# Kernel tuning notes

Hardware: AMD Instinct MI355X
Metric: run time of the kernel (lower is better)

The kernel has to match this reference:

```python
import jax, jax.numpy as jnp
import numpy as np

T, B, H, L = 1024, 64, 512, 2  # seq_len, batch, hidden(=input), num_layers


def setup_inputs() -> dict:
    key = jax.random.key(0)
    ks = jax.random.split(key, 9)
    std = 1.0 / np.sqrt(H)

    def u(k, shape):
        return jax.random.uniform(k, shape, jnp.float32, -std, std)

    x = jax.random.normal(ks[0], (T, B, H), jnp.float32)
    # per-direction stacked params: weights [L, 4H, in], biases [L, 4H]
    Wxh_f = u(ks[1], (L, 4 * H, H)); bxh_f = u(ks[2], (L, 4 * H))
    Whh_f = u(ks[3], (L, 4 * H, H)); bhh_f = u(ks[4], (L, 4 * H))
    Wxh_b = u(ks[5], (L, 4 * H, H)); bxh_b = u(ks[6], (L, 4 * H))
    Whh_b = u(ks[7], (L, 4 * H, H)); bhh_b = u(ks[8], (L, 4 * H))
    # LSTMCell.reset_parameters sets forget-gate bias chunk to 1/H
    fg = 1.0 / H
    bxh_f = bxh_f.at[:, H:2 * H].set(fg); bhh_f = bhh_f.at[:, H:2 * H].set(fg)
    bxh_b = bxh_b.at[:, H:2 * H].set(fg); bhh_b = bhh_b.at[:, H:2 * H].set(fg)
    return {"x": x,
            "Wxh_f": Wxh_f, "bxh_f": bxh_f, "Whh_f": Whh_f, "bhh_f": bhh_f,
            "Wxh_b": Wxh_b, "bxh_b": bxh_b, "Whh_b": Whh_b, "bhh_b": bhh_b}


def _run_direction(x, Wxh, bxh, Whh, bhh, reverse):
    # x: [T, B, in]; stacked L-layer LSTM scan in one direction.
    seq = x
    hs, cs = [], []
    for l in range(L):
        Wx, bx, Wh, bh = Wxh[l], bxh[l], Whh[l], bhh[l]

        def step(carry, xt):
            h, c = carry
            g = xt @ Wx.T + bx + h @ Wh.T + bh  # [B, 4H]
            i, f, gc, o = jnp.split(g, 4, axis=-1)  # chunk order: i, f, c, o
            c2 = jax.nn.sigmoid(f) * c + jax.nn.sigmoid(i) * jnp.tanh(gc)
            h2 = jax.nn.sigmoid(o) * jnp.tanh(c2)
            return (h2, c2), h2

        z = jnp.zeros((x.shape[1], H), x.dtype)
        (h, c), seq = jax.lax.scan(step, (z, z), seq, reverse=reverse)
        hs.append(h); cs.append(c)
    return seq, jnp.stack(hs), jnp.stack(cs)  # [T,B,H], [L,B,H], [L,B,H]


def reference(x, Wxh_f, bxh_f, Whh_f, bhh_f, Wxh_b, bxh_b, Whh_b, bhh_b):
    out_f, h_f, c_f = _run_direction(x, Wxh_f, bxh_f, Whh_f, bhh_f, reverse=False)
    out_b, h_b, c_b = _run_direction(x, Wxh_b, bxh_b, Whh_b, bhh_b, reverse=True)
    output = jnp.concatenate([out_f, out_b], axis=-1)  # [T, B, 2H]
    hidden = jnp.concatenate([h_f, h_b], axis=0)       # [2L, B, H]
    cell = jnp.concatenate([c_f, c_b], axis=0)         # [2L, B, H]
    return (output, hidden, cell)
```

## Files before the change

kernel.cpp:

```cpp
#include <hip/hip_runtime.h>
#include <hip/hip_bf16.h>


typedef __hip_bfloat16 bf16;
typedef short bf16x8 __attribute__((ext_vector_type(8)));
typedef float f32x4 __attribute__((ext_vector_type(4)));
typedef unsigned long long u64;

constexpr int T = 1024, B = 64, H = 512, G4 = 2048;
constexpr int W = 16;
constexpr int NW = 64;
constexpr int FSTRIDE = 16;
constexpr int ESTRIDE = 16;
constexpr size_t OUT_ELEMS = (size_t)T * B * 1024;
constexpr size_t HID_OFF   = OUT_ELEMS;
constexpr size_t CELL_OFF  = OUT_ELEMS + (size_t)4 * B * H;

__device__ __align__(256) unsigned g_flags[4 * NW * FSTRIDE];
__device__ __align__(256) unsigned g_epoch[4 * ESTRIDE];
__device__ __align__(256) bf16 g_ring [2 * W * B * H];
__device__ __align__(256) bf16 g_ring2[2 * W * B * H];

__global__ void init_ctrs() {
  const int i = blockIdx.x * blockDim.x + threadIdx.x;
  if (i < 4 * NW * FSTRIDE) g_flags[i] = 0;
  if (i < 4 * ESTRIDE)      g_epoch[i] = 0;
}

__device__ __forceinline__ bf16x8 cvt8(const float* p) {
  const float4 u = *(const float4*)p;
  const float4 v = *(const float4*)(p + 4);
  union { bf16 h[8]; bf16x8 r; } o;
  o.h[0] = __float2bfloat16(u.x); o.h[1] = __float2bfloat16(u.y);
  o.h[2] = __float2bfloat16(u.z); o.h[3] = __float2bfloat16(u.w);
  o.h[4] = __float2bfloat16(v.x); o.h[5] = __float2bfloat16(v.y);
  o.h[6] = __float2bfloat16(v.z); o.h[7] = __float2bfloat16(v.w);
  return o.r;
}

__device__ __forceinline__ bf16x8 ld16_dev(const bf16* p) {
  union { u64 u[2]; bf16x8 v; } r;
  r.u[0] = __hip_atomic_load((const u64*)p,     __ATOMIC_RELAXED,
                             __HIP_MEMORY_SCOPE_AGENT);
  r.u[1] = __hip_atomic_load((const u64*)p + 1, __ATOMIC_RELAXED,
                             __HIP_MEMORY_SCOPE_AGENT);
  return r.v;
}

__device__ __forceinline__ void st2_dev(bf16* p, float x) {
  const bf16 h = (bf16)x;
  unsigned short u;
  __builtin_memcpy(&u, &h, 2);
  __hip_atomic_store((unsigned short*)p, u, __ATOMIC_RELAXED,
                     __HIP_MEMORY_SCOPE_AGENT);
}

__device__ __forceinline__ void wave_poll(const unsigned* base, int lane,
                                          unsigned tgt) {
  const unsigned* p = base + lane * FSTRIDE;
  for (;;) {
    unsigned v = __hip_atomic_load(p, __ATOMIC_RELAXED,
                                   __HIP_MEMORY_SCOPE_AGENT);
    if (__all((int)(v >= tgt))) break;
    __builtin_amdgcn_s_sleep(1);
  }
}

__device__ __forceinline__ void poll_ge(const unsigned* p, unsigned tgt) {
  while (__hip_atomic_load(p, __ATOMIC_RELAXED,
                           __HIP_MEMORY_SCOPE_AGENT) < tgt)
    __builtin_amdgcn_s_sleep(1);
}

__global__ void __launch_bounds__(256, 1)
lstm_bidir(const float* __restrict__ x,
           const float* Wxf, const float* bxf, const float* Whf, const float* bhf,
           const float* Wxb, const float* bxb, const float* Whb, const float* bhb,
           float* out)
{
  __shared__ bf16 Wl[32 * 1024];

  const int tid   = threadIdx.x;
  const int bid   = blockIdx.x;
  const int stage = bid & 3;
  const int wg    = bid >> 2;
  const int dir   = stage & 1;
  const int layer = stage >> 1;
  const int c0    = wg * 8;

  const float* Wx = dir ? Wxb : Wxf;
  const float* Wh = dir ? Whb : Whf;
  const float* bx = dir ? bxb : bxf;
  const float* bh = dir ? bhb : bhf;
  bf16* ring  = g_ring  + (size_t)dir * W * B * H;
  bf16* ring2 = g_ring2 + (size_t)dir * W * B * H;

  for (int c = tid; c < 32 * 128; c += 256) {
    const int n  = c >> 7;
    const int kb = c & 127;
    const int ke = kb * 8;
    const int j = n >> 2, g = n & 3;
    const size_t row = (size_t)layer * G4 + (size_t)g * H + (c0 + j);
    const float* src = (ke < H) ? (Wx + row * H + ke) : (Wh + row * H + (ke - H));
    bf16x8 wv = cvt8(src);
    *(bf16x8*)(Wl + n * 1024 + ((kb ^ (n & 7)) * 8)) = wv;
  }

  const int lane = tid & 63, wi = tid >> 6;
  const int quad = lane >> 4, mr = lane & 15;
  const int g2 = wi & 1;
  const int mh = wi >> 1;
  const int nb = g2 * 16 + mr;
  const int j  = nb >> 2, gg = nb & 3;
  const int sw = nb & 7;

  const size_t brow = (size_t)layer * G4 + (size_t)gg * H + (c0 + j);
  const float bias = bx[brow] + bh[brow];

  __syncthreads();

  float cst[2][4] = {};
  unsigned nrounds = 0;
  unsigned*       myflags   = g_flags + stage * NW * FSTRIDE;
  unsigned*       myepoch   = g_epoch + stage * ESTRIDE;
  const unsigned* prodepoch = g_epoch + dir * ESTRIDE;
  const unsigned* consepoch = g_epoch + (2 + dir) * ESTRIDE;

  const int r0 = (stage < 2) ? 0 : 1;
  for (int r = r0; r < r0 + T; ++r) {
    int t;
    if (stage == 0)      t = r;
    else if (stage == 1) t = (T - 1) - r;
    else if (stage == 2) t = r - 1;
    else                 t = T - r;

    const bool first = dir ? (t == T - 1) : (t == 0);
    const bool last  = dir ? (t == 0) : (t == T - 1);

    const float* xf = nullptr;
    const bf16 *xsb = nullptr;
    const bf16 *hsrc; bf16* hdst_bf; float* hdst_f32 = nullptr;
    if (stage < 2) {
      xf      = x    + (size_t)t * B * H;
      hsrc    = ring + (size_t)((r - 1) & (W - 1)) * B * H;
      hdst_bf = ring + (size_t)(r & (W - 1)) * B * H;
    } else {
      xsb      = ring  + (size_t)((r - 1) & (W - 1)) * B * H;
      hsrc     = ring2 + (size_t)((r - 1) & (W - 1)) * B * H;
      hdst_bf  = ring2 + (size_t)(r & (W - 1)) * B * H;
      hdst_f32 = out + (size_t)t * B * 1024 + (size_t)dir * H;
    }

    f32x4 acc0 = {0.f, 0.f, 0.f, 0.f};
    f32x4 acc1 = {0.f, 0.f, 0.f, 0.f};
    const int arow = mh * 32 + mr;

    if (stage < 2) {
      #pragma unroll
      for (int kk = 0; kk < 16; ++kk) {
        const int blk = kk * 4 + quad;
        bf16x8 bfr = *(const bf16x8*)(Wl + nb * 1024 + ((blk ^ sw) * 8));
        const float* ap = xf + (size_t)arow * H + blk * 8;
        bf16x8 a0 = cvt8(ap);
        bf16x8 a1 = cvt8(ap + (size_t)16 * H);
        acc0 = __builtin_amdgcn_mfma_f32_16x16x32_bf16(a0, bfr, acc0, 0, 0, 0);
        acc1 = __builtin_amdgcn_mfma_f32_16x16x32_bf16(a1, bfr, acc1, 0, 0, 0);
      }
      if (tid < 64) {
        if (wg == 0) {
          wave_poll(myflags, tid, nrounds);
          if (tid == 0) {
            __hip_atomic_store(myepoch, nrounds, __ATOMIC_RELAXED,
                               __HIP_MEMORY_SCOPE_AGENT);
            if (r >= W) poll_ge(consepoch, (unsigned)(r - W + 1));
          }
        } else if (tid == 0) {
          poll_ge(myepoch, nrounds);
          if (r >= W) poll_ge(consepoch, (unsigned)(r - W + 1));
        }
      }
      __syncthreads();
      if (!first) {
        #pragma unroll
        for (int kk = 0; kk < 16; ++kk) {
          const int blk = 64 + kk * 4 + quad;
          bf16x8 bfr = *(const bf16x8*)(Wl + nb * 1024 + ((blk ^ sw) * 8));
          const bf16* ap = hsrc + (size_t)arow * H + (kk * 4 + quad) * 8;
          bf16x8 a0 = ld16_dev(ap);
          bf16x8 a1 = ld16_dev(ap + (size_t)16 * H);
          acc0 = __builtin_amdgcn_mfma_f32_16x16x32_bf16(a0, bfr, acc0, 0, 0, 0);
          acc1 = __builtin_amdgcn_mfma_f32_16x16x32_bf16(a1, bfr, acc1, 0, 0, 0);
        }
      }
    } else {
      if (tid == 0) poll_ge(prodepoch, (unsigned)r);
      __syncthreads();
      #pragma unroll
      for (int kk = 0; kk < 16; ++kk) {
        const int blk = kk * 4 + quad;
        bf16x8 bfr = *(const bf16x8*)(Wl + nb * 1024 + ((blk ^ sw) * 8));
        const bf16* ap = xsb + (size_t)arow * H + blk * 8;
        bf16x8 a0 = ld16_dev(ap);
        bf16x8 a1 = ld16_dev(ap + (size_t)16 * H);
        acc0 = __builtin_amdgcn_mfma_f32_16x16x32_bf16(a0, bfr, acc0, 0, 0, 0);
        acc1 = __builtin_amdgcn_mfma_f32_16x16x32_bf16(a1, bfr, acc1, 0, 0, 0);
      }
      if (tid < 64) {
        if (wg == 0) {
          wave_poll(myflags, tid, nrounds);
          if (tid == 0)
            __hip_atomic_store(myepoch, nrounds, __ATOMIC_RELAXED,
                               __HIP_MEMORY_SCOPE_AGENT);
        } else if (tid == 0) {
          poll_ge(myepoch, nrounds);
        }
      }
      __syncthreads();
      if (!first) {
        #pragma unroll
        for (int kk = 0; kk < 16; ++kk) {
          const int blk = 64 + kk * 4 + quad;
          bf16x8 bfr = *(const bf16x8*)(Wl + nb * 1024 + ((blk ^ sw) * 8));
          const bf16* ap = hsrc + (size_t)arow * H + (kk * 4 + quad) * 8;
          bf16x8 a0 = ld16_dev(ap);
          bf16x8 a1 = ld16_dev(ap + (size_t)16 * H);
          acc0 = __builtin_amdgcn_mfma_f32_16x16x32_bf16(a0, bfr, acc0, 0, 0, 0);
          acc1 = __builtin_amdgcn_mfma_f32_16x16x32_bf16(a1, bfr, acc1, 0, 0, 0);
        }
      }
    }

    #pragma unroll
    for (int m = 0; m < 2; ++m) {
      const f32x4 av = m ? acc1 : acc0;
      #pragma unroll
      for (int rr = 0; rr < 4; ++rr) {
        const float v  = av[rr] + bias;
        const float v1 = __shfl_xor(v, 1);
        const float v2 = __shfl_xor(v, 2);
        const float v3 = __shfl_xor(v, 3);
        float gi, gf, gc, go;
        if (gg == 0)      { gi = v;  gf = v1; gc = v2; go = v3; }
        else if (gg == 1) { gi = v1; gf = v;  gc = v3; go = v2; }
        else if (gg == 2) { gi = v2; gf = v3; gc = v;  go = v1; }
        else              { gi = v3; gf = v2; gc = v1; go = v;  }
        const float si = 1.f / (1.f + __expf(-gi));
        const float sf = 1.f / (1.f + __expf(-gf));
        const float so = 1.f / (1.f + __expf(-go));
        const float tc = 1.f - 2.f / (1.f + __expf(2.f * gc));
        const float c2 = sf * cst[m][rr] + si * tc;
        cst[m][rr] = c2;
        const float th = 1.f - 2.f / (1.f + __expf(2.f * c2));
        const float hv = so * th;
        if (gg == 0) {
          const int b = mh * 32 + m * 16 + quad * 4 + rr;
          st2_dev(hdst_bf + (size_t)b * H + (c0 + j), hv);
          if (stage >= 2) hdst_f32[(size_t)b * 1024 + (c0 + j)] = hv;
          if (last) {
            const size_t p = (size_t)(dir * 2 + layer) * (B * H) + (size_t)b * H + (c0 + j);
            out[HID_OFF + p]  = hv;
            out[CELL_OFF + p] = c2;
          }
        }
      }
    }

    asm volatile("s_waitcnt vmcnt(0)" ::: "memory");
    __syncthreads();
    ++nrounds;
    if (tid == 0) {
      __hip_atomic_store(myflags + wg * FSTRIDE, nrounds,
                         __ATOMIC_RELAXED, __HIP_MEMORY_SCOPE_AGENT);
    }
  }

  if (wg == 0 && tid < 64) {
    wave_poll(myflags, tid, (unsigned)T);
    if (tid == 0)
      __hip_atomic_store(myepoch, (unsigned)T, __ATOMIC_RELAXED,
                         __HIP_MEMORY_SCOPE_AGENT);
  }
}

extern "C" void kernel_launch(void* const* d_in, const int* in_sizes, int n_in,
                              void* d_out, int out_size, void* d_ws, size_t ws_size,
                              hipStream_t stream) {
  const float* x   = (const float*)d_in[0];
  const float* Wxf = (const float*)d_in[1];
  const float* bxf = (const float*)d_in[2];
  const float* Whf = (const float*)d_in[3];
  const float* bhf = (const float*)d_in[4];
  const float* Wxb = (const float*)d_in[5];
  const float* bxb = (const float*)d_in[6];
  const float* Whb = (const float*)d_in[7];
  const float* bhb = (const float*)d_in[8];
  float* out = (float*)d_out;

  hipLaunchKernelGGL(init_ctrs, dim3(16), dim3(256), 0, stream);
  hipLaunchKernelGGL(lstm_bidir, dim3(256), dim3(256), 0, stream,
                     x, Wxf, bxf, Whf, bhf, Wxb, bxb, Whb, bhb, out);
}
```

Before: 18.92 ms.

## Prefetch ring loads in register batches and coalesce h stores via shared memory

Replaces the per-iteration load-then-MFMA loops with a helper that issues ring-buffer loads in batches of four k-steps into double-buffered registers, so global load latency overlaps the MFMAs. The hidden-state outputs are no longer written as scattered 2-byte atomic stores from each lane. They are staged in a small shared array and then written by one wave as 16-byte bf16 rows plus float4 rows for the f32 output. This cuts the number of tiny global stores on the per-step critical path, at the cost of an extra barrier and higher register pressure.

```diff
diff --git a/kernel.cpp b/kernel.cpp
--- a/kernel.cpp
+++ b/kernel.cpp
@@ -47,14 +47,6 @@
   return r.v;
 }
 
-__device__ __forceinline__ void st2_dev(bf16* p, float x) {
-  const bf16 h = (bf16)x;
-  unsigned short u;
-  __builtin_memcpy(&u, &h, 2);
-  __hip_atomic_store((unsigned short*)p, u, __ATOMIC_RELAXED,
-                     __HIP_MEMORY_SCOPE_AGENT);
-}
-
 __device__ __forceinline__ void wave_poll(const unsigned* base, int lane,
                                           unsigned tgt) {
   const unsigned* p = base + lane * FSTRIDE;
@@ -72,6 +64,52 @@
     __builtin_amdgcn_s_sleep(1);
 }
 
+template<int WBASE>
+__device__ __forceinline__ void ring_gemm(const bf16* abase,
+                                          const bf16* Wl, int nb, int sw,
+                                          int quad, f32x4& acc0, f32x4& acc1) {
+  bf16x8 P0[4], P1[4], Q0[4], Q1[4];
+  #pragma unroll
+  for (int u = 0; u < 4; ++u) {
+    const int blk = u * 4 + quad;
+    P0[u] = ld16_dev(abase + blk * 8);
+    P1[u] = ld16_dev(abase + (size_t)16 * H + blk * 8);
+  }
+  #pragma unroll
+  for (int u = 0; u < 4; ++u) {
+    const int blk = (4 + u) * 4 + quad;
+    Q0[u] = ld16_dev(abase + blk * 8);
+    Q1[u] = ld16_dev(abase + (size_t)16 * H + blk * 8);
+  }
+  #pragma unroll
+  for (int g = 0; g < 4; ++g) {
+    #pragma unroll
+    for (int u = 0; u < 4; ++u) {
+      const int kk   = g * 4 + u;
+      const int wblk = WBASE + kk * 4 + quad;
+      bf16x8 bfr = *(const bf16x8*)(Wl + nb * 1024 + ((wblk ^ sw) * 8));
+      bf16x8 a0 = (g & 1) ? Q0[u] : P0[u];
+      bf16x8 a1 = (g & 1) ? Q1[u] : P1[u];
+      acc0 = __builtin_amdgcn_mfma_f32_16x16x32_bf16(a0, bfr, acc0, 0, 0, 0);
+      acc1 = __builtin_amdgcn_mfma_f32_16x16x32_bf16(a1, bfr, acc1, 0, 0, 0);
+    }
+    if (g < 2) {
+      #pragma unroll
+      for (int u = 0; u < 4; ++u) {
+        const int kk2 = (g + 2) * 4 + u;
+        const int blk = kk2 * 4 + quad;
+        if (g & 1) {
+          Q0[u] = ld16_dev(abase + blk * 8);
+          Q1[u] = ld16_dev(abase + (size_t)16 * H + blk * 8);
+        } else {
+          P0[u] = ld16_dev(abase + blk * 8);
+          P1[u] = ld16_dev(abase + (size_t)16 * H + blk * 8);
+        }
+      }
+    }
+  }
+}
+
 __global__ void __launch_bounds__(256, 1)
 lstm_bidir(const float* __restrict__ x,
            const float* Wxf, const float* bxf, const float* Whf, const float* bhf,
@@ -79,6 +117,7 @@
            float* out)
 {
   __shared__ bf16 Wl[32 * 1024];
+  __shared__ float sh[64][8];
 
   const int tid   = threadIdx.x;
   const int bid   = blockIdx.x;
@@ -180,31 +219,12 @@
         }
       }
       __syncthreads();
-      if (!first) {
-        #pragma unroll
-        for (int kk = 0; kk < 16; ++kk) {
-          const int blk = 64 + kk * 4 + quad;
-          bf16x8 bfr = *(const bf16x8*)(Wl + nb * 1024 + ((blk ^ sw) * 8));
-          const bf16* ap = hsrc + (size_t)arow * H + (kk * 4 + quad) * 8;
-          bf16x8 a0 = ld16_dev(ap);
-          bf16x8 a1 = ld16_dev(ap + (size_t)16 * H);
-          acc0 = __builtin_amdgcn_mfma_f32_16x16x32_bf16(a0, bfr, acc0, 0, 0, 0);
-          acc1 = __builtin_amdgcn_mfma_f32_16x16x32_bf16(a1, bfr, acc1, 0, 0, 0);
-        }
-      }
+      if (!first)
+        ring_gemm<64>(hsrc + (size_t)arow * H, Wl, nb, sw, quad, acc0, acc1);
     } else {
       if (tid == 0) poll_ge(prodepoch, (unsigned)r);
       __syncthreads();
-      #pragma unroll
-      for (int kk = 0; kk < 16; ++kk) {
-        const int blk = kk * 4 + quad;
-        bf16x8 bfr = *(const bf16x8*)(Wl + nb * 1024 + ((blk ^ sw) * 8));
-        const bf16* ap = xsb + (size_t)arow * H + blk * 8;
-        bf16x8 a0 = ld16_dev(ap);
-        bf16x8 a1 = ld16_dev(ap + (size_t)16 * H);
-        acc0 = __builtin_amdgcn_mfma_f32_16x16x32_bf16(a0, bfr, acc0, 0, 0, 0);
-        acc1 = __builtin_amdgcn_mfma_f32_16x16x32_bf16(a1, bfr, acc1, 0, 0, 0);
-      }
+      ring_gemm<0>(xsb + (size_t)arow * H, Wl, nb, sw, quad, acc0, acc1);
       if (tid < 64) {
         if (wg == 0) {
           wave_poll(myflags, tid, nrounds);
@@ -216,18 +236,8 @@
         }
       }
       __syncthreads();
-      if (!first) {
-        #pragma unroll
-        for (int kk = 0; kk < 16; ++kk) {
-          const int blk = 64 + kk * 4 + quad;
-          bf16x8 bfr = *(const bf16x8*)(Wl + nb * 1024 + ((blk ^ sw) * 8));
-          const bf16* ap = hsrc + (size_t)arow * H + (kk * 4 + quad) * 8;
-          bf16x8 a0 = ld16_dev(ap);
-          bf16x8 a1 = ld16_dev(ap + (size_t)16 * H);
-          acc0 = __builtin_amdgcn_mfma_f32_16x16x32_bf16(a0, bfr, acc0, 0, 0, 0);
-          acc1 = __builtin_amdgcn_mfma_f32_16x16x32_bf16(a1, bfr, acc1, 0, 0, 0);
-        }
-      }
+      if (!first)
+        ring_gemm<64>(hsrc + (size_t)arow * H, Wl, nb, sw, quad, acc0, acc1);
     }
 
     #pragma unroll
@@ -254,8 +264,7 @@
         const float hv = so * th;
         if (gg == 0) {
           const int b = mh * 32 + m * 16 + quad * 4 + rr;
-          st2_dev(hdst_bf + (size_t)b * H + (c0 + j), hv);
-          if (stage >= 2) hdst_f32[(size_t)b * 1024 + (c0 + j)] = hv;
+          sh[b][j] = hv;
           if (last) {
             const size_t p = (size_t)(dir * 2 + layer) * (B * H) + (size_t)b * H + (c0 + j);
             out[HID_OFF + p]  = hv;
@@ -265,7 +274,28 @@
       }
     }
 
-    asm volatile("s_waitcnt vmcnt(0)" ::: "memory");
+    __syncthreads();
+    if (tid < 64) {
+      const int b = tid;
+      const float4 u0 = *(const float4*)&sh[b][0];
+      const float4 u1 = *(const float4*)&sh[b][4];
+      union { bf16 h[8]; u64 q[2]; } o;
+      o.h[0] = __float2bfloat16(u0.x); o.h[1] = __float2bfloat16(u0.y);
+      o.h[2] = __float2bfloat16(u0.z); o.h[3] = __float2bfloat16(u0.w);
+      o.h[4] = __float2bfloat16(u1.x); o.h[5] = __float2bfloat16(u1.y);
+      o.h[6] = __float2bfloat16(u1.z); o.h[7] = __float2bfloat16(u1.w);
+      bf16* rp = hdst_bf + (size_t)b * H + c0;
+      __hip_atomic_store((u64*)rp,     o.q[0], __ATOMIC_RELAXED,
+                         __HIP_MEMORY_SCOPE_AGENT);
+      __hip_atomic_store((u64*)rp + 1, o.q[1], __ATOMIC_RELAXED,
+                         __HIP_MEMORY_SCOPE_AGENT);
+      if (stage >= 2) {
+        float* op = hdst_f32 + (size_t)b * 1024 + c0;
+        *(float4*)op       = u0;
+        *(float4*)(op + 4) = u1;
+      }
+      asm volatile("s_waitcnt vmcnt(0)" ::: "memory");
+    }
     __syncthreads();
     ++nrounds;
     if (tid == 0) {
```

Measured after the change: 18.96 ms. About the same (+0.2%).
